# Kernel optimization log

Measured on AMD Instinct MI355X. Metric: run time of the kernel, lower is better.

Reference implementation:

```python
import jax, jax.numpy as jnp
import numpy as np

POOL = 7
IMAGE_SHAPE = (1024, 1024, 3)


def _crop_and_resize(fmap, boxes, pool):
    """TF-style crop_and_resize with extrapolation_value=0.
    fmap: [C, H, W]; boxes: [N, (y1,x1,y2,x2)] normalized. Returns [N, C, pool, pool]."""
    C, H, W = fmap.shape
    dt = fmap.dtype
    y1, x1, y2, x2 = boxes[:, 0], boxes[:, 1], boxes[:, 2], boxes[:, 3]
    g = jnp.arange(pool, dtype=dt) / (pool - 1)  # [P] in [0,1]
    ys = (y1[:, None] + g[None, :] * (y2 - y1)[:, None]) * (H - 1)  # [N,P]
    xs = (x1[:, None] + g[None, :] * (x2 - x1)[:, None]) * (W - 1)  # [N,P]
    y0f = jnp.floor(ys); x0f = jnp.floor(xs)
    ly = (ys - y0f).astype(dt); lx = (xs - x0f).astype(dt)
    y0 = jnp.clip(y0f.astype(jnp.int32), 0, H - 1)
    y1i = jnp.clip(y0 + 1, 0, H - 1)
    x0 = jnp.clip(x0f.astype(jnp.int32), 0, W - 1)
    x1i = jnp.clip(x0 + 1, 0, W - 1)
    vy = ((ys >= 0) & (ys <= H - 1)).astype(dt)  # extrapolation_value = 0 outside
    vx = ((xs >= 0) & (xs <= W - 1)).astype(dt)

    def at(yi, xi):
        # gather -> [C, N, P, P]
        return fmap[:, yi[:, :, None], xi[:, None, :]]

    wy0 = (1 - ly)[None, :, :, None]; wy1 = ly[None, :, :, None]
    wx0 = (1 - lx)[None, :, None, :]; wx1 = lx[None, :, None, :]
    val = (at(y0, x0) * wy0 + at(y1i, x0) * wy1) * wx0 \
        + (at(y0, x1i) * wy0 + at(y1i, x1i) * wy1) * wx1
    val = val * (vy[None, :, :, None] * vx[None, :, None, :])
    return jnp.transpose(val, (1, 0, 2, 3))  # [N, C, P, P]


def reference(boxes, p2, p3, p4, p5):
    """pyramid_roi_align: route each box to FPN level 2..5 via the 224-scale
    log2 heuristic, then CropAndResize(pool, pool, 0) from that level.
    Output order matches input box order (original sorts back by box_to_level)."""
    h = boxes[:, 2] - boxes[:, 0]
    w = boxes[:, 3] - boxes[:, 1]
    image_area = float(IMAGE_SHAPE[0] * IMAGE_SHAPE[1])
    roi_level = 4.0 + jnp.log2(jnp.sqrt(h * w) / (224.0 / np.sqrt(image_area)))
    roi_level = jnp.clip(jnp.round(roi_level).astype(jnp.int32), 2, 5)
    boxes_d = jax.lax.stop_gradient(boxes)  # level_boxes.detach() in original
    fmaps = [p2, p3, p4, p5]
    pooled = jnp.zeros((boxes.shape[0], p2.shape[0], POOL, POOL), dtype=p2.dtype)
    for i, level in enumerate(range(2, 6)):
        mask = (roi_level == level).astype(p2.dtype)[:, None, None, None]
        pooled = pooled + mask * _crop_and_resize(fmaps[i], boxes_d, POOL)
    return pooled


def setup_inputs():
    key = jax.random.key(0)
    kb, ks, k2, k3, k4, k5 = jax.random.split(key, 6)
    N, C = 1000, 256
    size = jax.random.uniform(ks, (N, 2), minval=0.02, maxval=0.9)
    tl = jax.random.uniform(kb, (N, 2)) * (1.0 - size)  # top-left so box stays in [0,1]
    boxes = jnp.concatenate([tl[:, 0:1], tl[:, 1:2],
                             tl[:, 0:1] + size[:, 0:1], tl[:, 1:2] + size[:, 1:2]], axis=1)
    p2 = jax.random.normal(k2, (C, 256, 256), jnp.float32)
    p3 = jax.random.normal(k3, (C, 128, 128), jnp.float32)
    p4 = jax.random.normal(k4, (C, 64, 64), jnp.float32)
    p5 = jax.random.normal(k5, (C, 32, 32), jnp.float32)
    return {"boxes": boxes, "p2": p2, "p3": p3, "p4": p4, "p5": p5}
```

## Files before the change

kernel.cpp:

```cpp
#include <hip/hip_runtime.h>


#define POOL 7
#define NCH  256
#define ELEMS_PER_BOX (NCH * POOL * POOL)
#define CHUNKS 7
#define CHUNK_ELEMS (ELEMS_PER_BOX / CHUNKS)

typedef float f2 __attribute__((ext_vector_type(2)));

__global__ __launch_bounds__(256) void roi_align_kernel(
    const float* __restrict__ boxes,
    const float* __restrict__ p2, const float* __restrict__ p3,
    const float* __restrict__ p4, const float* __restrict__ p5,
    float* __restrict__ out, int N)
{
    const int bid   = blockIdx.x;
    const int n     = bid % N;
    const int chunk = bid / N;

    __shared__ int   s_off0[49], s_off1[49];
    __shared__ float s_a[49], s_b[49];
    __shared__ float s_w0[49], s_w1[49];
    __shared__ int   s_HW;
    __shared__ const float* s_fmap;

    const int tid = threadIdx.x;

    if (tid < 49) {
        const float by1 = boxes[4 * n + 0];
        const float bx1 = boxes[4 * n + 1];
        const float by2 = boxes[4 * n + 2];
        const float bx2 = boxes[4 * n + 3];
        const float h = by2 - by1;
        const float w = bx2 - bx1;
        float rl = 4.0f + log2f(sqrtf(h * w) / 0.21875f);
        int level = (int)rintf(rl);
        level = min(5, max(2, level));
        const int H = 256 >> (level - 2);
        const int W = H;
        if (tid == 0) {
            s_HW = H * W;
            s_fmap = (level == 2) ? p2 : (level == 3) ? p3 : (level == 4) ? p4 : p5;
        }
        const int py = tid / 7;
        const int px = tid - 7 * py;

        const float ty = (float)py / (float)(POOL - 1);
        const float ys = (by1 + ty * (by2 - by1)) * (float)(H - 1);
        const float yf = floorf(ys);
        const float ly = ys - yf;
        int y0 = (int)yf; y0 = min(H - 1, max(0, y0));
        const int y1 = min(H - 1, y0 + 1);
        const float vy = (ys >= 0.0f && ys <= (float)(H - 1)) ? 1.0f : 0.0f;

        const float tx = (float)px / (float)(POOL - 1);
        const float xs = (bx1 + tx * (bx2 - bx1)) * (float)(W - 1);
        const float xf = floorf(xs);
        const float lx = xs - xf;
        int x0 = (int)xf; x0 = min(W - 1, max(0, x0));
        const float vx = (xs >= 0.0f && xs <= (float)(W - 1)) ? 1.0f : 0.0f;

        const int xb = min(x0, W - 2);
        const bool edge = (x0 != xb);
        const float a = edge ? 0.0f : vx * (1.0f - lx);
        const float b = edge ? vx : vx * lx;

        s_off0[tid] = y0 * W + xb;
        s_off1[tid] = y1 * W + xb;
        s_a[tid] = a;
        s_b[tid] = b;
        s_w0[tid] = vy * (1.0f - ly);
        s_w1[tid] = vy * ly;
    }
    __syncthreads();

    const float* __restrict__ fmap = s_fmap;
    const int HW = s_HW;

    const int i0 = chunk * CHUNK_ELEMS + tid;
    int c  = i0 / 49;
    int pp = i0 - c * 49;

    f2  q0[CHUNKS], q1[CHUNKS];
    int cell[CHUNKS];
    {
        int cc = c, p = pp;
#pragma unroll
        for (int k = 0; k < CHUNKS; ++k) {
            cell[k] = p;
            const float* plane = fmap + (size_t)cc * HW;
            q0[k] = *(const f2*)(plane + s_off0[p]);
            q1[k] = *(const f2*)(plane + s_off1[p]);
            cc += 5; p += 11;
            if (p >= 49) { p -= 49; cc += 1; }
        }
    }

    float* __restrict__ obase = out + (size_t)n * ELEMS_PER_BOX + chunk * CHUNK_ELEMS;
#pragma unroll
    for (int k = 0; k < CHUNKS; ++k) {
        const int p = cell[k];
        const float a = s_a[p], b = s_b[p];
        const float r0 = q0[k].x * a + q0[k].y * b;
        const float r1 = q1[k].x * a + q1[k].y * b;
        obase[tid + k * 256] = r0 * s_w0[p] + r1 * s_w1[p];
    }
}

extern "C" void kernel_launch(void* const* d_in, const int* in_sizes, int n_in,
                              void* d_out, int out_size, void* d_ws, size_t ws_size,
                              hipStream_t stream) {
    const float* boxes = (const float*)d_in[0];
    const float* p2    = (const float*)d_in[1];
    const float* p3    = (const float*)d_in[2];
    const float* p4    = (const float*)d_in[3];
    const float* p5    = (const float*)d_in[4];
    float* out = (float*)d_out;
    const int N = in_sizes[0] / 4;

    roi_align_kernel<<<N * CHUNKS, 256, 0, stream>>>(boxes, p2, p3, p4, p5, out, N);
}
```

Before: 142.0 us.

## Stage box row segments in LDS with coalesced float4 loads per channel group

```diff
diff --git a/kernel.cpp b/kernel.cpp
--- a/kernel.cpp
+++ b/kernel.cpp
@@ -4,25 +4,33 @@
 #define POOL 7
 #define NCH  256
 #define ELEMS_PER_BOX (NCH * POOL * POOL)
-#define CHUNKS 7
-#define CHUNK_ELEMS (ELEMS_PER_BOX / CHUNKS)
+#define HALF_ELEMS (ELEMS_PER_BOX / 2)
+#define CG 8
+#define NGROUPS 16
+#define ROWS 14
+#define SA 32
+#define SROW 36
+#define GROUP_OUT (CG * 49)
 
 typedef float f2 __attribute__((ext_vector_type(2)));
+typedef float f4 __attribute__((ext_vector_type(4)));
 
-__global__ __launch_bounds__(256) void roi_align_kernel(
+__global__ __launch_bounds__(256, 8) void roi_align_kernel(
     const float* __restrict__ boxes,
     const float* __restrict__ p2, const float* __restrict__ p3,
     const float* __restrict__ p4, const float* __restrict__ p5,
     float* __restrict__ out, int N)
 {
-    const int bid   = blockIdx.x;
-    const int n     = bid % N;
-    const int chunk = bid / N;
+    const int bid  = blockIdx.x;
+    const int n    = bid >> 1;
+    const int half = bid & 1;
 
+    __shared__ float s_stage[CG * ROWS * SROW];
+    __shared__ float s_a[49], s_b[49], s_w0[49], s_w1[49];
+    __shared__ int   s_dx[49];
     __shared__ int   s_off0[49], s_off1[49];
-    __shared__ float s_a[49], s_b[49];
-    __shared__ float s_w0[49], s_w1[49];
-    __shared__ int   s_HW;
+    __shared__ int   s_rowoff[ROWS];
+    __shared__ int   s_HW, s_xb0a, s_sa4, s_fast;
     __shared__ const float* s_fmap;
 
     const int tid = threadIdx.x;
@@ -39,14 +47,10 @@
         level = min(5, max(2, level));
         const int H = 256 >> (level - 2);
         const int W = H;
-        if (tid == 0) {
-            s_HW = H * W;
-            s_fmap = (level == 2) ? p2 : (level == 3) ? p3 : (level == 4) ? p4 : p5;
-        }
         const int py = tid / 7;
         const int px = tid - 7 * py;
 
-        const float ty = (float)py / (float)(POOL - 1);
+        const float ty = (float)py / 6.0f;
         const float ys = (by1 + ty * (by2 - by1)) * (float)(H - 1);
         const float yf = floorf(ys);
         const float ly = ys - yf;
@@ -54,17 +58,25 @@
         const int y1 = min(H - 1, y0 + 1);
         const float vy = (ys >= 0.0f && ys <= (float)(H - 1)) ? 1.0f : 0.0f;
 
-        const float tx = (float)px / (float)(POOL - 1);
+        const float tx = (float)px / 6.0f;
         const float xs = (bx1 + tx * (bx2 - bx1)) * (float)(W - 1);
         const float xf = floorf(xs);
         const float lx = xs - xf;
         int x0 = (int)xf; x0 = min(W - 1, max(0, x0));
         const float vx = (xs >= 0.0f && xs <= (float)(W - 1)) ? 1.0f : 0.0f;
-
         const int xb = min(x0, W - 2);
         const bool edge = (x0 != xb);
         const float a = edge ? 0.0f : vx * (1.0f - lx);
         const float b = edge ? vx : vx * lx;
+
+        const float xsA = (bx1 + 0.0f * (bx2 - bx1)) * (float)(W - 1);
+        int xA = (int)floorf(xsA); xA = min(W - 1, max(0, xA));
+        const int xbA = min(xA, W - 2);
+        const float xsB = (bx1 + 1.0f * (bx2 - bx1)) * (float)(W - 1);
+        int xB = (int)floorf(xsB); xB = min(W - 1, max(0, xB));
+        const int xbB = min(xB, W - 2);
+        const int xb0a = min(xbA & ~3, W - SA);
+        const int need = xbB + 2 - xb0a;
 
         s_off0[tid] = y0 * W + xb;
         s_off1[tid] = y1 * W + xb;
@@ -72,39 +84,100 @@
         s_b[tid] = b;
         s_w0[tid] = vy * (1.0f - ly);
         s_w1[tid] = vy * ly;
+        s_dx[tid] = xb - xb0a;
+        if (px == 0) {
+            s_rowoff[2 * py]     = y0 * W;
+            s_rowoff[2 * py + 1] = y1 * W;
+        }
+        if (tid == 0) {
+            s_HW = H * W;
+            s_fmap = (level == 2) ? p2 : (level == 3) ? p3 : (level == 4) ? p4 : p5;
+            s_xb0a = xb0a;
+            s_sa4  = (need + 3) >> 2;
+            s_fast = (need <= SA) ? 1 : 0;
+        }
     }
     __syncthreads();
 
-    const float* __restrict__ fmap = s_fmap;
     const int HW = s_HW;
+    const float* __restrict__ fbase = s_fmap + (size_t)(half * 128) * HW;
+    float* __restrict__ op = out + (size_t)n * ELEMS_PER_BOX + half * HALF_ELEMS;
 
-    const int i0 = chunk * CHUNK_ELEMS + tid;
-    int c  = i0 / 49;
-    int pp = i0 - c * 49;
+    const int c1  = tid / 49,  p1  = tid - 49 * c1;
+    const int o2  = 256 + tid;
+    const int c2  = o2 / 49,   p2i = o2 - 49 * c2;
+    const bool act2 = (tid < GROUP_OUT - 256);
 
-    f2  q0[CHUNKS], q1[CHUNKS];
-    int cell[CHUNKS];
-    {
-        int cc = c, p = pp;
+    const float a1 = s_a[p1],  b1 = s_b[p1],  w01 = s_w0[p1],  w11 = s_w1[p1];
+    const float a2 = s_a[p2i], b2 = s_b[p2i], w02 = s_w0[p2i], w12 = s_w1[p2i];
+
+    if (s_fast) {
+        const int sa4  = s_sa4;
+        const int xb0a = s_xb0a;
+
+        int goff[4], lw[4];
+        bool gact[4];
 #pragma unroll
-        for (int k = 0; k < CHUNKS; ++k) {
-            cell[k] = p;
-            const float* plane = fmap + (size_t)cc * HW;
-            q0[k] = *(const f2*)(plane + s_off0[p]);
-            q1[k] = *(const f2*)(plane + s_off1[p]);
-            cc += 5; p += 11;
-            if (p >= 49) { p -= 49; cc += 1; }
+        for (int pp = 0; pp < 4; ++pp) {
+            const int idx = pp * 256 + tid;
+            const int rid = idx >> 3;
+            const int q   = idx & 7;
+            gact[pp] = (rid < CG * ROWS) && (q < sa4);
+            const int cl = rid / 14;
+            const int r  = rid - 14 * cl;
+            lw[pp]   = rid * SROW + q * 4;
+            goff[pp] = cl * HW + s_rowoff[r] + xb0a + q * 4;
         }
-    }
 
-    float* __restrict__ obase = out + (size_t)n * ELEMS_PER_BOX + chunk * CHUNK_ELEMS;
+        const int t1 = (c1 * ROWS + 2 * (p1 / 7)) * SROW + s_dx[p1];
+        const int t2 = (c2 * ROWS + 2 * (p2i / 7)) * SROW + s_dx[p2i];
+
+        for (int g = 0; g < NGROUPS; ++g) {
+            const float* fg = fbase + (size_t)(g * CG) * HW;
+            f4 v[4];
 #pragma unroll
-    for (int k = 0; k < CHUNKS; ++k) {
-        const int p = cell[k];
-        const float a = s_a[p], b = s_b[p];
-        const float r0 = q0[k].x * a + q0[k].y * b;
-        const float r1 = q1[k].x * a + q1[k].y * b;
-        obase[tid + k * 256] = r0 * s_w0[p] + r1 * s_w1[p];
+            for (int pp = 0; pp < 4; ++pp)
+                if (gact[pp]) v[pp] = *(const f4*)(fg + goff[pp]);
+#pragma unroll
+            for (int pp = 0; pp < 4; ++pp)
+                if (gact[pp]) *(f4*)(&s_stage[lw[pp]]) = v[pp];
+            __syncthreads();
+
+            {
+                const float t00 = s_stage[t1],        t01 = s_stage[t1 + 1];
+                const float t10 = s_stage[t1 + SROW], t11 = s_stage[t1 + SROW + 1];
+                const float r0 = t00 * a1 + t01 * b1;
+                const float r1 = t10 * a1 + t11 * b1;
+                op[g * GROUP_OUT + tid] = r0 * w01 + r1 * w11;
+            }
+            if (act2) {
+                const float u00 = s_stage[t2],        u01 = s_stage[t2 + 1];
+                const float u10 = s_stage[t2 + SROW], u11 = s_stage[t2 + SROW + 1];
+                const float s0 = u00 * a2 + u01 * b2;
+                const float s1 = u10 * a2 + u11 * b2;
+                op[g * GROUP_OUT + 256 + tid] = s0 * w02 + s1 * w12;
+            }
+            __syncthreads();
+        }
+    } else {
+        const int off01 = s_off0[p1],  off11 = s_off1[p1];
+        const int off02 = s_off0[p2i], off12 = s_off1[p2i];
+        for (int g = 0; g < NGROUPS; ++g) {
+            const float* pl1 = fbase + (size_t)(g * CG + c1) * HW;
+            const f2 q0 = *(const f2*)(pl1 + off01);
+            const f2 q1 = *(const f2*)(pl1 + off11);
+            const float r0 = q0.x * a1 + q0.y * b1;
+            const float r1 = q1.x * a1 + q1.y * b1;
+            op[g * GROUP_OUT + tid] = r0 * w01 + r1 * w11;
+            if (act2) {
+                const float* pl2 = fbase + (size_t)(g * CG + c2) * HW;
+                const f2 u0 = *(const f2*)(pl2 + off02);
+                const f2 u1 = *(const f2*)(pl2 + off12);
+                const float s0 = u0.x * a2 + u0.y * b2;
+                const float s1 = u1.x * a2 + u1.y * b2;
+                op[g * GROUP_OUT + 256 + tid] = s0 * w02 + s1 * w12;
+            }
+        }
     }
 }
 
@@ -119,5 +192,5 @@
     float* out = (float*)d_out;
     const int N = in_sizes[0] / 4;
 
-    roi_align_kernel<<<N * CHUNKS, 256, 0, stream>>>(boxes, p2, p3, p4, p5, out, N);
+    roi_align_kernel<<<N * 2, 256, 0, stream>>>(boxes, p2, p3, p4, p5, out, N);
 }
```

New measurement: 169.2 us. 1.19x slower.

## Pair adjacent pool cells into shared 4-wide gathers per row

Applied to the files above, without the earlier changes.

```diff
diff --git a/kernel.cpp b/kernel.cpp
--- a/kernel.cpp
+++ b/kernel.cpp
@@ -4,12 +4,16 @@
 #define POOL 7
 #define NCH  256
 #define ELEMS_PER_BOX (NCH * POOL * POOL)
+#define UNITS 28
+#define BOX_UNITS (NCH * UNITS)
 #define CHUNKS 7
-#define CHUNK_ELEMS (ELEMS_PER_BOX / CHUNKS)
-
-typedef float f2 __attribute__((ext_vector_type(2)));
-
-__global__ __launch_bounds__(256) void roi_align_kernel(
+#define CHUNK_UNITS (BOX_UNITS / CHUNKS)
+#define ITERS (CHUNK_UNITS / 256)
+
+typedef float f2  __attribute__((ext_vector_type(2), aligned(4)));
+typedef float f4u __attribute__((ext_vector_type(4), aligned(4)));
+
+__global__ __launch_bounds__(256, 4) void roi_align_kernel(
     const float* __restrict__ boxes,
     const float* __restrict__ p2, const float* __restrict__ p3,
     const float* __restrict__ p4, const float* __restrict__ p5,
@@ -19,11 +23,17 @@
     const int n     = bid % N;
     const int chunk = bid / N;
 
-    __shared__ int   s_off0[49], s_off1[49];
-    __shared__ float s_a[49], s_b[49];
-    __shared__ float s_w0[49], s_w1[49];
-    __shared__ int   s_HW;
+    __shared__ float s_a[49], s_b[49], s_w0[49], s_w1[49];
+    __shared__ int   s_x0[49];
+    __shared__ int   s_r0[7], s_r1[7];
+    __shared__ int   s_HW, s_W;
     __shared__ const float* s_fmap;
+    __shared__ int    s_uoff0[28], s_uoff1[28];
+    __shared__ int    s_woff0[28], s_woff1[28];
+    __shared__ int    s_meta[28];
+    __shared__ float  s_uw0[28], s_uw1[28];
+    __shared__ float  s_aB[28], s_bB[28];
+    __shared__ float4 s_wA4[28], s_wB4[28];
 
     const int tid = threadIdx.x;
 
@@ -39,14 +49,10 @@
         level = min(5, max(2, level));
         const int H = 256 >> (level - 2);
         const int W = H;
-        if (tid == 0) {
-            s_HW = H * W;
-            s_fmap = (level == 2) ? p2 : (level == 3) ? p3 : (level == 4) ? p4 : p5;
-        }
         const int py = tid / 7;
         const int px = tid - 7 * py;
 
-        const float ty = (float)py / (float)(POOL - 1);
+        const float ty = (float)py / 6.0f;
         const float ys = (by1 + ty * (by2 - by1)) * (float)(H - 1);
         const float yf = floorf(ys);
         const float ly = ys - yf;
@@ -54,57 +60,129 @@
         const int y1 = min(H - 1, y0 + 1);
         const float vy = (ys >= 0.0f && ys <= (float)(H - 1)) ? 1.0f : 0.0f;
 
-        const float tx = (float)px / (float)(POOL - 1);
+        const float tx = (float)px / 6.0f;
         const float xs = (bx1 + tx * (bx2 - bx1)) * (float)(W - 1);
         const float xf = floorf(xs);
         const float lx = xs - xf;
         int x0 = (int)xf; x0 = min(W - 1, max(0, x0));
         const float vx = (xs >= 0.0f && xs <= (float)(W - 1)) ? 1.0f : 0.0f;
-
         const int xb = min(x0, W - 2);
         const bool edge = (x0 != xb);
         const float a = edge ? 0.0f : vx * (1.0f - lx);
         const float b = edge ? vx : vx * lx;
 
-        s_off0[tid] = y0 * W + xb;
-        s_off1[tid] = y1 * W + xb;
-        s_a[tid] = a;
-        s_b[tid] = b;
+        s_x0[tid] = xb;
+        s_a[tid]  = a;
+        s_b[tid]  = b;
         s_w0[tid] = vy * (1.0f - ly);
         s_w1[tid] = vy * ly;
+        if (px == 0) { s_r0[py] = y0 * W; s_r1[py] = y1 * W; }
+        if (tid == 0) {
+            s_HW = H * W;
+            s_W  = W;
+            s_fmap = (level == 2) ? p2 : (level == 3) ? p3 : (level == 4) ? p4 : p5;
+        }
     }
     __syncthreads();
 
-    const float* __restrict__ fmap = s_fmap;
+    if (tid < 28) {
+        const int W  = s_W;
+        const int py = tid >> 2;
+        const int xu = tid & 3;
+        const int pA = py * 7 + 2 * xu;
+        const bool pair = (xu < 3);
+        const int x0A = s_x0[pA];
+        const int x0B = pair ? s_x0[pA + 1] : x0A;
+        const int xq  = min(x0A, W - 4);
+        const int dA  = x0A - xq;
+        const int dB  = x0B - xq;
+        const bool wide = pair && (dB > 2);
+        const float aA = s_a[pA], bA = s_b[pA];
+        const float aB = pair ? s_a[pA + 1] : 0.0f;
+        const float bB = pair ? s_b[pA + 1] : 0.0f;
+
+        float4 wa, wb;
+        wa.x = (dA == 0) ? aA : 0.0f;
+        wa.y = (dA == 0) ? bA : ((dA == 1) ? aA : 0.0f);
+        wa.z = (dA == 1) ? bA : ((dA == 2) ? aA : 0.0f);
+        wa.w = (dA == 2) ? bA : 0.0f;
+        const bool nb = pair && !wide;
+        wb.x = (nb && dB == 0) ? aB : 0.0f;
+        wb.y = nb ? ((dB == 0) ? bB : ((dB == 1) ? aB : 0.0f)) : 0.0f;
+        wb.z = nb ? ((dB == 1) ? bB : ((dB == 2) ? aB : 0.0f)) : 0.0f;
+        wb.w = (nb && dB == 2) ? bB : 0.0f;
+
+        s_uoff0[tid] = s_r0[py] + xq;
+        s_uoff1[tid] = s_r1[py] + xq;
+        s_woff0[tid] = wide ? (s_r0[py] + x0B) : -1;
+        s_woff1[tid] = wide ? (s_r1[py] + x0B) : -1;
+        s_meta[tid]  = pA | (pair ? 0x100 : 0);
+        s_uw0[tid] = s_w0[pA];
+        s_uw1[tid] = s_w1[pA];
+        s_aB[tid] = aB;
+        s_bB[tid] = bB;
+        s_wA4[tid] = wa;
+        s_wB4[tid] = wb;
+    }
+    __syncthreads();
+
     const int HW = s_HW;
-
-    const int i0 = chunk * CHUNK_ELEMS + tid;
-    int c  = i0 / 49;
-    int pp = i0 - c * 49;
-
-    f2  q0[CHUNKS], q1[CHUNKS];
-    int cell[CHUNKS];
+    const float* __restrict__ lvl = s_fmap;
+    float* __restrict__ obase = out + (size_t)n * ELEMS_PER_BOX;
+
+    const int flat0 = chunk * CHUNK_UNITS + tid;
+    const int c0 = flat0 / 28;
+    const int u0 = flat0 - 28 * c0;
+
+    f4u q0[ITERS], q1[ITERS];
+    f2  e0[ITERS], e1[ITERS];
+    int cc[ITERS], uu[ITERS];
     {
-        int cc = c, p = pp;
+        int c_ = c0, u_ = u0;
 #pragma unroll
-        for (int k = 0; k < CHUNKS; ++k) {
-            cell[k] = p;
-            const float* plane = fmap + (size_t)cc * HW;
-            q0[k] = *(const f2*)(plane + s_off0[p]);
-            q1[k] = *(const f2*)(plane + s_off1[p]);
-            cc += 5; p += 11;
-            if (p >= 49) { p -= 49; cc += 1; }
+        for (int k = 0; k < ITERS; ++k) {
+            cc[k] = c_; uu[k] = u_;
+            const float* pl = lvl + (size_t)c_ * HW;
+            q0[k] = *(const f4u*)(pl + s_uoff0[u_]);
+            q1[k] = *(const f4u*)(pl + s_uoff1[u_]);
+            const int wo0 = s_woff0[u_];
+            if (wo0 >= 0) {
+                e0[k] = *(const f2*)(pl + wo0);
+                e1[k] = *(const f2*)(pl + s_woff1[u_]);
+            }
+            c_ += 9; u_ += 4;
+            if (u_ >= 28) { u_ -= 28; c_ += 1; }
         }
     }
 
-    float* __restrict__ obase = out + (size_t)n * ELEMS_PER_BOX + chunk * CHUNK_ELEMS;
 #pragma unroll
-    for (int k = 0; k < CHUNKS; ++k) {
-        const int p = cell[k];
-        const float a = s_a[p], b = s_b[p];
-        const float r0 = q0[k].x * a + q0[k].y * b;
-        const float r1 = q1[k].x * a + q1[k].y * b;
-        obase[tid + k * 256] = r0 * s_w0[p] + r1 * s_w1[p];
+    for (int k = 0; k < ITERS; ++k) {
+        const int u_ = uu[k];
+        const float w0u = s_uw0[u_], w1u = s_uw1[u_];
+        const float4 wa = s_wA4[u_];
+        const float r0 = q0[k].x * wa.x + q0[k].y * wa.y +
+                         q0[k].z * wa.z + q0[k].w * wa.w;
+        const float r1 = q1[k].x * wa.x + q1[k].y * wa.y +
+                         q1[k].z * wa.z + q1[k].w * wa.w;
+        const int meta = s_meta[u_];
+        float* op = obase + cc[k] * 49 + (meta & 0xff);
+        op[0] = r0 * w0u + r1 * w1u;
+        if (meta & 0x100) {
+            float oB;
+            if (s_woff0[u_] >= 0) {
+                const float aB = s_aB[u_], bB = s_bB[u_];
+                oB = (e0[k].x * aB + e0[k].y * bB) * w0u +
+                     (e1[k].x * aB + e1[k].y * bB) * w1u;
+            } else {
+                const float4 wb = s_wB4[u_];
+                const float s0 = q0[k].x * wb.x + q0[k].y * wb.y +
+                                 q0[k].z * wb.z + q0[k].w * wb.w;
+                const float s1 = q1[k].x * wb.x + q1[k].y * wb.y +
+                                 q1[k].z * wb.z + q1[k].w * wb.w;
+                oB = s0 * w0u + s1 * w1u;
+            }
+            op[1] = oB;
+        }
     }
 }
 
```

New measurement: 148.1 us. 1.04x slower.
